# Kernel tuning notes

Hardware: AMD Instinct MI355X
Metric: run time of the kernel (lower is better)

## Reference

```python
import jax, jax.numpy as jnp
import numpy as np

NUM_NODES = 8192
MUL = 64
ENV_P = 6
EPSILON = 1.0 / np.sqrt(17.0)  # 1/sqrt(1 + avg_num_neighbors), avg_num_neighbors=16


def _envelope(u, p=ENV_P):
    # polynomial smoothing envelope (cutoff at u = 1)
    a = -(p + 1) * (p + 2) / 2.0
    b = p * (p + 2)
    c = -p * (p + 1) / 2.0
    f = 1.0 + a * u ** p + b * u ** (p + 1) + c * u ** (p + 2)
    return jnp.where(u < 1.0, f, 0.0)


def setup_inputs() -> dict:
    key = jax.random.key(0)
    ks = jax.random.split(key, 9)
    E, F = 131072, 512
    vectors = jax.random.normal(ks[0], (E, 3), jnp.float32) * 0.35  # mostly inside cutoff
    x = jax.random.normal(ks[1], (E, F), jnp.float32)
    V = jax.random.normal(ks[2], (E, MUL, 4), jnp.float32)  # per mul-channel: [0e | 1o(3)]
    senders = jax.random.randint(ks[3], (E,), 0, NUM_NODES, jnp.int32)
    W_w = jax.random.normal(ks[4], (F, MUL), jnp.float32)
    W1 = jax.random.normal(ks[5], (F + 2 * MUL, 512), jnp.float32)
    W2 = jax.random.normal(ks[6], (512, 512), jnp.float32)
    W3 = jax.random.normal(ks[7], (512, 512), jnp.float32)
    W_lin = jax.random.normal(ks[8], (3 * MUL, MUL), jnp.float32)
    return {"vectors": vectors, "x": x, "V": V, "senders": senders,
            "W_w": W_w, "W1": W1, "W2": W2, "W3": W3, "W_lin": W_lin}


def reference(vectors, x, V, senders, W_w, W1, W2, W3, W_lin):
    E = vectors.shape[0]
    # edge-wise linear producing tensor-product weights  [E, MUL]
    w = (x @ W_w) / np.sqrt(x.shape[-1])
    # spherical harmonics (component norm), l = 0..1 of normalized vectors -> [E, 4]
    r = jnp.linalg.norm(vectors, axis=-1, keepdims=True)          # [E, 1]
    nhat = vectors / r
    Y = jnp.concatenate([jnp.ones((E, 1), vectors.dtype), np.sqrt(3.0) * nhat], axis=1)
    # weighted SH, scatter-sum over senders, gather back (map_back=True), scale by epsilon
    wY_e = w[:, :, None] * Y[:, None, :]                          # [E, MUL, 4]
    agg = jax.ops.segment_sum(wY_e, senders, num_segments=NUM_NODES)
    wY = agg[senders] * EPSILON                                   # [E, MUL, 4]
    # CG tensor product wY (0e+1o) x V (0e+1o), keep 0e and 1o outputs
    a0, a1 = wY[..., 0], wY[..., 1:]
    b0, b1 = V[..., 0], V[..., 1:]
    scal = jnp.concatenate(
        [a0 * b0, jnp.einsum('emi,emi->em', a1, b1) / np.sqrt(3.0)], axis=-1)  # [E, 2*MUL]
    vecs = jnp.concatenate(
        [a0[..., None] * b1, a1 * b0[..., None], jnp.cross(a1, b1) / np.sqrt(2.0)],
        axis=1)                                                   # [E, 3*MUL, 3]
    # concat scalar channel into invariants, 3-layer MLP (silu, linear last)
    xc = jnp.concatenate([x, scal], axis=1)                       # [E, 640]
    h = jax.nn.silu(xc @ W1 / np.sqrt(xc.shape[-1]))
    h = jax.nn.silu(h @ W2 / np.sqrt(h.shape[-1]))
    h = h @ W3 / np.sqrt(h.shape[-1])
    x_out = _envelope(r) * h                                      # [E, 512]
    # equivariant linear over the 1o multiplicity axis
    V_out = jnp.einsum('ekc,km->emc', vecs, W_lin) / np.sqrt(vecs.shape[1])  # [E, MUL, 3]
    return x_out, V_out
```

## Files before the change

kernel.cpp:

```cpp
#include <hip/hip_runtime.h>
#include <cstdint>
#include <cstddef>

#define E_TOT 131072
#define NNODES 8192

typedef __attribute__((ext_vector_type(8))) short bf16x8;
typedef __attribute__((ext_vector_type(4))) float f32x4;
typedef unsigned short u16;
typedef unsigned int u32;

__device__ __forceinline__ u16 f2bf(float f) {
    u32 u = __builtin_bit_cast(u32, f);
    u32 r = (u + 0x7FFFu + ((u >> 16) & 1u)) >> 16;
    return (u16)r;
}

__device__ __forceinline__ void gload16(const u16* g, u16* l) {
    __builtin_amdgcn_global_load_lds((const __attribute__((address_space(1))) void*)g,
                                     (__attribute__((address_space(3))) void*)l, 16, 0, 0);
}

__device__ __forceinline__ bf16x8 lds_frag(const u16* base, int row, int bytecol) {
    return *(const bf16x8*)((const char*)base + row * 128 + (bytecol ^ ((row & 7) << 4)));
}

__global__ void wconv_kernel(const float* __restrict__ src, u16* __restrict__ dst,
                             int K, int N) {
    int idx = blockIdx.x * 256 + threadIdx.x;
    if (idx >= N * K) return;
    int n = idx / K, k = idx - n * K;
    dst[idx] = f2bf(src[(size_t)k * N + n]);
}

__global__ void xconv_kernel(const float4* __restrict__ x, ushort4* __restrict__ xb) {
    size_t i = (size_t)blockIdx.x * 256 + threadIdx.x;
    float4 v = x[i];
    ushort4 o;
    o.x = f2bf(v.x); o.y = f2bf(v.y); o.z = f2bf(v.z); o.w = f2bf(v.w);
    xb[i] = o;
}

__global__ void envy_kernel(const float* __restrict__ vectors, float* __restrict__ env,
                            float4* __restrict__ Y) {
    int e = blockIdx.x * 256 + threadIdx.x;
    float vx = vectors[3 * e + 0], vy = vectors[3 * e + 1], vz = vectors[3 * e + 2];
    float r2 = vx * vx + vy * vy + vz * vz;
    float r = sqrtf(r2);
    float u6 = r2 * r2 * r2;
    float f = 1.0f + u6 * (-28.0f + 48.0f * r - 21.0f * r2);
    env[e] = (r < 1.0f) ? f : 0.0f;
    float inv = 1.7320508075688772f / r;
    Y[e] = make_float4(1.0f, vx * inv, vy * inv, vz * inv);
}

__global__ void hist_kernel(const int* __restrict__ senders, int* __restrict__ cnt) {
    int e = blockIdx.x * 256 + threadIdx.x;
    atomicAdd(&cnt[senders[e]], 1);
}

__launch_bounds__(1024)
__global__ void scan_kernel(const int* __restrict__ cnt, int* __restrict__ off,
                            int* __restrict__ curs) {
    __shared__ int part[1024];
    const int t = threadIdx.x;
    int local[8];
    int s = 0;
#pragma unroll
    for (int j = 0; j < 8; ++j) { local[j] = cnt[t * 8 + j]; s += local[j]; }
    part[t] = s;
    __syncthreads();
    for (int d = 1; d < 1024; d <<= 1) {
        int v = (t >= d) ? part[t - d] : 0;
        __syncthreads();
        part[t] += v;
        __syncthreads();
    }
    int run = part[t] - s;
#pragma unroll
    for (int j = 0; j < 8; ++j) {
        off[t * 8 + j] = run;
        curs[t * 8 + j] = run;
        run += local[j];
    }
    if (t == 1023) off[8192] = run;
}

__global__ void permbuild_kernel(const int* __restrict__ senders, int* __restrict__ curs,
                                 int* __restrict__ perm) {
    int e = blockIdx.x * 256 + threadIdx.x;
    int s = senders[e];
    int p = atomicAdd(&curs[s], 1);
    perm[p] = e;
}

__launch_bounds__(256)
__global__ void gather_kernel(const float* __restrict__ w, const float4* __restrict__ Y,
                              const int* __restrict__ off, const int* __restrict__ perm,
                              float4* __restrict__ agg) {
    const int t = threadIdx.x;
    const int n = blockIdx.x * 4 + (t >> 6);
    const int m = t & 63;
    const int beg = off[n], end = off[n + 1];
    float4 acc = make_float4(0.f, 0.f, 0.f, 0.f);
    for (int i = beg; i < end; ++i) {
        int e = perm[i];
        float wv = w[(size_t)e * 64 + m];
        float4 y = Y[e];
        acc.x += wv * y.x; acc.y += wv * y.y; acc.z += wv * y.z; acc.w += wv * y.w;
    }
    agg[(size_t)n * 64 + m] = acc;
}

__launch_bounds__(256)
__global__ void wgemm_kernel(const u16* __restrict__ XB, const u16* __restrict__ Wt,
                             float* __restrict__ w) {
    __shared__ u16 As[128 * 72];
    __shared__ u16 Bs[64 * 72];
    const int e0 = blockIdx.x * 128;
    const int t = threadIdx.x, lane = t & 63, wid = t >> 6;
    const int lr = lane & 15, lh = lane >> 4;
    const int r8 = t >> 3, c8 = t & 7;
    f32x4 acc[2][4] = {};
    for (int kt = 0; kt < 8; ++kt) {
        const int kk = kt << 6;
#pragma unroll
        for (int i = 0; i < 4; ++i) {
            int row = i * 32 + r8;
            const u16* g = XB + (size_t)(e0 + row) * 512 + kk + c8 * 8;
            *(uint4*)((char*)As + row * 144 + c8 * 16) = *(const uint4*)g;
        }
#pragma unroll
        for (int i = 0; i < 2; ++i) {
            int row = i * 32 + r8;
            const u16* g = Wt + (size_t)row * 512 + kk + c8 * 8;
            *(uint4*)((char*)Bs + row * 144 + c8 * 16) = *(const uint4*)g;
        }
        __syncthreads();
#pragma unroll
        for (int k2 = 0; k2 < 2; ++k2) {
            bf16x8 af[2], bfr[4];
#pragma unroll
            for (int m = 0; m < 2; ++m)
                af[m] = *(const bf16x8*)((const char*)As + (wid * 32 + m * 16 + lr) * 144 + k2 * 64 + lh * 16);
#pragma unroll
            for (int n = 0; n < 4; ++n)
                bfr[n] = *(const bf16x8*)((const char*)Bs + (n * 16 + lr) * 144 + k2 * 64 + lh * 16);
#pragma unroll
            for (int m = 0; m < 2; ++m)
#pragma unroll
                for (int n = 0; n < 4; ++n)
                    acc[m][n] = __builtin_amdgcn_mfma_f32_16x16x32_bf16(af[m], bfr[n], acc[m][n], 0, 0, 0);
        }
        __syncthreads();
    }
    const float s = 0.044194173824159216f;
#pragma unroll
    for (int m = 0; m < 2; ++m)
#pragma unroll
        for (int n = 0; n < 4; ++n)
#pragma unroll
            for (int j = 0; j < 4; ++j) {
                int e = e0 + wid * 32 + m * 16 + lh * 4 + j;
                w[(size_t)e * 64 + n * 16 + lr] = acc[m][n][j] * s;
            }
}

__launch_bounds__(256)
__global__ void edge_kernel(const int* __restrict__ senders, const float4* __restrict__ agg4,
                            const float4* __restrict__ V4, const u16* __restrict__ Wlt,
                            u16* __restrict__ scal, float* __restrict__ Vout) {
    __shared__ u16 a_lds[3][32][200];
    __shared__ u16 w_lds[64 * 200];
    const int t = threadIdx.x;
    const int e0 = blockIdx.x * 32;
#pragma unroll
    for (int i = 0; i < 6; ++i) {
        int c = i * 256 + t;
        int row = c / 24, off = (c % 24) * 8;
        *(uint4*)((char*)w_lds + row * 400 + off * 2) = ((const uint4*)Wlt)[c];
    }
    const float invs3 = 0.5773502691896258f;
    const float invs2 = 0.7071067811865476f;
    const float EPS = 0.24253562503633297f;
#pragma unroll
    for (int i = 0; i < 8; ++i) {
        int el = i * 4 + (t >> 6);
        int m = t & 63;
        int e = e0 + el;
        int s = senders[e];
        float4 a = agg4[(size_t)s * 64 + m];
        a.x *= EPS; a.y *= EPS; a.z *= EPS; a.w *= EPS;
        float4 b = V4[(size_t)e * 64 + m];
        float s0 = a.x * b.x;
        float s1 = (a.y * b.y + a.z * b.z + a.w * b.w) * invs3;
        scal[(size_t)e * 128 + m] = f2bf(s0);
        scal[(size_t)e * 128 + 64 + m] = f2bf(s1);
        float cx = (a.z * b.w - a.w * b.z) * invs2;
        float cy = (a.w * b.y - a.y * b.w) * invs2;
        float cz = (a.y * b.z - a.z * b.y) * invs2;
        a_lds[0][el][m] = f2bf(a.x * b.y);
        a_lds[0][el][64 + m] = f2bf(a.y * b.x);
        a_lds[0][el][128 + m] = f2bf(cx);
        a_lds[1][el][m] = f2bf(a.x * b.z);
        a_lds[1][el][64 + m] = f2bf(a.z * b.x);
        a_lds[1][el][128 + m] = f2bf(cy);
        a_lds[2][el][m] = f2bf(a.x * b.w);
        a_lds[2][el][64 + m] = f2bf(a.w * b.x);
        a_lds[2][el][128 + m] = f2bf(cz);
    }
    __syncthreads();
    const int lane = t & 63, wid = t >> 6;
    const int lr = lane & 15, lh = lane >> 4;
    f32x4 acc[3][2] = {};
    for (int kt = 0; kt < 6; ++kt) {
        bf16x8 bfr = *(const bf16x8*)((const char*)w_lds + (wid * 16 + lr) * 400 + kt * 64 + lh * 16);
#pragma unroll
        for (int c = 0; c < 3; ++c)
#pragma unroll
            for (int m = 0; m < 2; ++m) {
                bf16x8 afr = *(const bf16x8*)((const char*)a_lds + ((c * 32 + m * 16 + lr) * 400) + kt * 64 + lh * 16);
                acc[c][m] = __builtin_amdgcn_mfma_f32_16x16x32_bf16(afr, bfr, acc[c][m], 0, 0, 0);
            }
    }
    __syncthreads();
    float* ot = (float*)a_lds;
    const float sc = 0.07216878364870323f;
#pragma unroll
    for (int c = 0; c < 3; ++c)
#pragma unroll
        for (int m = 0; m < 2; ++m)
#pragma unroll
            for (int j = 0; j < 4; ++j) {
                int row = m * 16 + lh * 4 + j;
                int mul = wid * 16 + lr;
                ot[row * 192 + mul * 3 + c] = acc[c][m][j] * sc;
            }
    __syncthreads();
    float4* vo = (float4*)(Vout + (size_t)e0 * 192);
#pragma unroll
    for (int i = 0; i < 6; ++i)
        vo[i * 256 + t] = ((float4*)ot)[i * 256 + t];
}

template <int MODE>
__launch_bounds__(256)
__global__ void mlp_gemm(const u16* __restrict__ A, const u16* __restrict__ A2,
                         const u16* __restrict__ Bt, const int K, const float scale,
                         const float* __restrict__ env,
                         u16* __restrict__ outb, float* __restrict__ outf) {
    __shared__ u16 As[128 * 64];
    __shared__ u16 Bs[128 * 64];
    const int nwg = gridDim.x;
    const int bid = blockIdx.x;
    const int swz = (bid & 7) * (nwg >> 3) + (bid >> 3);
    const int mt = swz >> 2, nt = swz & 3;
    const int e0 = mt << 7, n0 = nt << 7;
    const int t = threadIdx.x, lane = t & 63, wid = t >> 6;
    const int wm = wid & 1, wn = wid >> 1;
    const int lr = lane & 15, lh = lane >> 4;
    f32x4 acc[4][4] = {};
    const int nkt = K >> 6;
    const int srow = wid * 8 + (lane >> 3);
    const int scol = ((lane & 7) ^ (lane >> 3)) * 8;
    for (int kt = 0; kt < nkt; ++kt) {
        const int kk = kt << 6;
        const int col = kk + scol;
#pragma unroll
        for (int i = 0; i < 4; ++i) {
            const int row = e0 + i * 32 + srow;
            const u16* g;
            if (A2 && kk >= 512) g = A2 + (size_t)row * 128 + (col - 512);
            else                 g = A + (size_t)row * 512 + col;
            gload16(g, As + i * 2048 + wid * 512);
        }
#pragma unroll
        for (int i = 0; i < 4; ++i) {
            const int row = n0 + i * 32 + srow;
            const u16* g = Bt + (size_t)row * K + col;
            gload16(g, Bs + i * 2048 + wid * 512);
        }
        __syncthreads();
#pragma unroll
        for (int k2 = 0; k2 < 2; ++k2) {
            bf16x8 af[4], bfr[4];
#pragma unroll
            for (int m = 0; m < 4; ++m)
                af[m] = lds_frag(As, wm * 64 + m * 16 + lr, k2 * 64 + lh * 16);
#pragma unroll
            for (int n = 0; n < 4; ++n)
                bfr[n] = lds_frag(Bs, wn * 64 + n * 16 + lr, k2 * 64 + lh * 16);
#pragma unroll
            for (int m = 0; m < 4; ++m)
#pragma unroll
                for (int n = 0; n < 4; ++n)
                    acc[m][n] = __builtin_amdgcn_mfma_f32_16x16x32_bf16(af[m], bfr[n], acc[m][n], 0, 0, 0);
        }
        __syncthreads();
    }
#pragma unroll
    for (int m = 0; m < 4; ++m) {
#pragma unroll
        for (int j = 0; j < 4; ++j) {
            const int row = e0 + wm * 64 + m * 16 + lh * 4 + j;
            float ev = (MODE == 1) ? env[row] : 0.0f;
#pragma unroll
            for (int n = 0; n < 4; ++n) {
                const int col = n0 + wn * 64 + n * 16 + lr;
                float v = acc[m][n][j] * scale;
                if (MODE == 0) {
                    float sv = v / (1.0f + __expf(-v));
                    outb[(size_t)row * 512 + col] = f2bf(sv);
                } else {
                    outf[(size_t)row * 512 + col] = v * ev;
                }
            }
        }
    }
}

extern "C" void kernel_launch(void* const* d_in, const int* in_sizes, int n_in,
                              void* d_out, int out_size, void* d_ws, size_t ws_size,
                              hipStream_t stream) {
    const float* vectors = (const float*)d_in[0];
    const float* x       = (const float*)d_in[1];
    const float* V       = (const float*)d_in[2];
    const int*   senders = (const int*)d_in[3];
    const float* W_w     = (const float*)d_in[4];
    const float* W1      = (const float*)d_in[5];
    const float* W2      = (const float*)d_in[6];
    const float* W3      = (const float*)d_in[7];
    const float* W_lin   = (const float*)d_in[8];
    float* out = (float*)d_out;
    char* ws = (char*)d_ws;

    u16*    XB   = (u16*)(ws + 0x0);
    u16*    H1   = (u16*)(ws + 0x8000000);
    u16*    SCAL = (u16*)(ws + 0x10000000);
    float*  AGG  = (float*)(ws + 0x12000000);
    float*  ENV  = (float*)(ws + 0x12800000);
    float4* Yb   = (float4*)(ws + 0x12880000);
    float*  Wbuf = (float*)(ws + 0x12A80000);
    u16*    WT   = (u16*)(ws + 0x14A80000);
    u16* Wwt = WT;
    u16* W1t = Wwt + 64 * 512;
    u16* W2t = W1t + 512 * 640;
    u16* W3t = W2t + 512 * 512;
    u16* Wlt = W3t + 512 * 512;
    u16* H2 = XB;
    int* COUNT = (int*)(ws + 0x15000000);
    int* OFF   = (int*)(ws + 0x15010000);
    int* CURS  = (int*)(ws + 0x15020000);
    int* PERM  = (int*)(ws + 0x15030000);

    hipMemsetAsync(COUNT, 0, NNODES * sizeof(int), stream);

    wconv_kernel<<<(64 * 512) / 256, 256, 0, stream>>>(W_w, Wwt, 512, 64);
    wconv_kernel<<<(512 * 640) / 256, 256, 0, stream>>>(W1, W1t, 640, 512);
    wconv_kernel<<<(512 * 512) / 256, 256, 0, stream>>>(W2, W2t, 512, 512);
    wconv_kernel<<<(512 * 512) / 256, 256, 0, stream>>>(W3, W3t, 512, 512);
    wconv_kernel<<<(64 * 192) / 256, 256, 0, stream>>>(W_lin, Wlt, 192, 64);

    xconv_kernel<<<(E_TOT * 512 / 4) / 256, 256, 0, stream>>>((const float4*)x, (ushort4*)XB);
    envy_kernel<<<E_TOT / 256, 256, 0, stream>>>(vectors, ENV, Yb);

    hist_kernel<<<E_TOT / 256, 256, 0, stream>>>(senders, COUNT);
    scan_kernel<<<1, 1024, 0, stream>>>(COUNT, OFF, CURS);
    permbuild_kernel<<<E_TOT / 256, 256, 0, stream>>>(senders, CURS, PERM);

    wgemm_kernel<<<E_TOT / 128, 256, 0, stream>>>(XB, Wwt, Wbuf);
    gather_kernel<<<NNODES / 4, 256, 0, stream>>>(Wbuf, Yb, OFF, PERM, (float4*)AGG);

    edge_kernel<<<E_TOT / 32, 256, 0, stream>>>(senders, (const float4*)AGG, (const float4*)V,
                                                Wlt, SCAL, out + (size_t)E_TOT * 512);

    const float s640 = 0.03952847075210474f;
    const float s512 = 0.044194173824159216f;
    mlp_gemm<0><<<(E_TOT / 128) * 4, 256, 0, stream>>>(XB, SCAL, W1t, 640, s640, nullptr, H1, nullptr);
    mlp_gemm<0><<<(E_TOT / 128) * 4, 256, 0, stream>>>(H1, nullptr, W2t, 512, s512, nullptr, H2, nullptr);
    mlp_gemm<1><<<(E_TOT / 128) * 4, 256, 0, stream>>>(H2, nullptr, W3t, 512, s512, ENV, nullptr, out);
}
```

Before: 650.8 us.

## Use 256x256 double-buffered tiles with 512 threads in MLP GEMMs

The three MLP GEMMs move from 128x128 tiles with 256 threads to 256x256 tiles with 512 threads (8 waves, each computing 128x64). LDS is double-buffered so the global-to-LDS loads for the next k-tile are issued before the MFMAs on the current one, leaving one barrier per iteration. The larger tile improves operand reuse and cuts global traffic per FLOP. In exchange it uses 128KB of LDS and 128 accumulator floats per lane, so occupancy drops, and the grid shrinks to 1024 blocks.

```diff
diff --git a/kernel.cpp b/kernel.cpp
--- a/kernel.cpp
+++ b/kernel.cpp
@@ -244,54 +244,71 @@
 }
 
 template <int MODE>
-__launch_bounds__(256)
+__launch_bounds__(512, 2)
 __global__ void mlp_gemm(const u16* __restrict__ A, const u16* __restrict__ A2,
                          const u16* __restrict__ Bt, const int K, const float scale,
                          const float* __restrict__ env,
                          u16* __restrict__ outb, float* __restrict__ outf) {
-    __shared__ u16 As[128 * 64];
-    __shared__ u16 Bs[128 * 64];
+    __shared__ u16 lds[2][2][256 * 64];
     const int nwg = gridDim.x;
     const int bid = blockIdx.x;
     const int swz = (bid & 7) * (nwg >> 3) + (bid >> 3);
-    const int mt = swz >> 2, nt = swz & 3;
-    const int e0 = mt << 7, n0 = nt << 7;
+    const int mt = swz >> 1, nt = swz & 1;
+    const int e0 = mt << 8, n0 = nt << 8;
     const int t = threadIdx.x, lane = t & 63, wid = t >> 6;
-    const int wm = wid & 1, wn = wid >> 1;
+    const int wm = wid >> 2, wn = wid & 3;
     const int lr = lane & 15, lh = lane >> 4;
-    f32x4 acc[4][4] = {};
+    const int sr8 = lane >> 3;
+    const int scol = ((lane & 7) ^ sr8) << 3;
+    f32x4 acc[8][4] = {};
     const int nkt = K >> 6;
-    const int srow = wid * 8 + (lane >> 3);
-    const int scol = ((lane & 7) ^ (lane >> 3)) * 8;
+
     for (int kt = 0; kt < nkt; ++kt) {
-        const int kk = kt << 6;
-        const int col = kk + scol;
-#pragma unroll
-        for (int i = 0; i < 4; ++i) {
-            const int row = e0 + i * 32 + srow;
-            const u16* g;
-            if (A2 && kk >= 512) g = A2 + (size_t)row * 128 + (col - 512);
-            else                 g = A + (size_t)row * 512 + col;
-            gload16(g, As + i * 2048 + wid * 512);
-        }
-#pragma unroll
-        for (int i = 0; i < 4; ++i) {
-            const int row = n0 + i * 32 + srow;
-            const u16* g = Bt + (size_t)row * K + col;
-            gload16(g, Bs + i * 2048 + wid * 512);
-        }
-        __syncthreads();
+        if (kt == 0) {
+            const int col = scol;
+#pragma unroll
+            for (int i = 0; i < 4; ++i) {
+                const int row = e0 + i * 64 + wid * 8 + sr8;
+                gload16(A + (size_t)row * 512 + col, &lds[0][0][i * 4096 + wid * 512]);
+            }
+#pragma unroll
+            for (int i = 0; i < 4; ++i) {
+                const int row = n0 + i * 64 + wid * 8 + sr8;
+                gload16(Bt + (size_t)row * K + col, &lds[0][1][i * 4096 + wid * 512]);
+            }
+            __syncthreads();
+        }
+        if (kt + 1 < nkt) {
+            const int kk = (kt + 1) << 6;
+            const int col = kk + scol;
+            const int nb = (kt + 1) & 1;
+#pragma unroll
+            for (int i = 0; i < 4; ++i) {
+                const int row = e0 + i * 64 + wid * 8 + sr8;
+                const u16* g;
+                if (A2 && kk >= 512) g = A2 + (size_t)row * 128 + (col - 512);
+                else                 g = A + (size_t)row * 512 + col;
+                gload16(g, &lds[nb][0][i * 4096 + wid * 512]);
+            }
+#pragma unroll
+            for (int i = 0; i < 4; ++i) {
+                const int row = n0 + i * 64 + wid * 8 + sr8;
+                gload16(Bt + (size_t)row * K + col, &lds[nb][1][i * 4096 + wid * 512]);
+            }
+        }
+        const u16* Ab = lds[kt & 1][0];
+        const u16* Bb = lds[kt & 1][1];
 #pragma unroll
         for (int k2 = 0; k2 < 2; ++k2) {
-            bf16x8 af[4], bfr[4];
-#pragma unroll
-            for (int m = 0; m < 4; ++m)
-                af[m] = lds_frag(As, wm * 64 + m * 16 + lr, k2 * 64 + lh * 16);
+            bf16x8 af[8], bfr[4];
+#pragma unroll
+            for (int m = 0; m < 8; ++m)
+                af[m] = lds_frag(Ab, wm * 128 + m * 16 + lr, k2 * 64 + lh * 16);
 #pragma unroll
             for (int n = 0; n < 4; ++n)
-                bfr[n] = lds_frag(Bs, wn * 64 + n * 16 + lr, k2 * 64 + lh * 16);
-#pragma unroll
-            for (int m = 0; m < 4; ++m)
+                bfr[n] = lds_frag(Bb, wn * 64 + n * 16 + lr, k2 * 64 + lh * 16);
+#pragma unroll
+            for (int m = 0; m < 8; ++m)
 #pragma unroll
                 for (int n = 0; n < 4; ++n)
                     acc[m][n] = __builtin_amdgcn_mfma_f32_16x16x32_bf16(af[m], bfr[n], acc[m][n], 0, 0, 0);
@@ -299,10 +316,10 @@
         __syncthreads();
     }
 #pragma unroll
-    for (int m = 0; m < 4; ++m) {
+    for (int m = 0; m < 8; ++m) {
 #pragma unroll
         for (int j = 0; j < 4; ++j) {
-            const int row = e0 + wm * 64 + m * 16 + lh * 4 + j;
+            const int row = e0 + wm * 128 + m * 16 + lh * 4 + j;
             float ev = (MODE == 1) ? env[row] : 0.0f;
 #pragma unroll
             for (int n = 0; n < 4; ++n) {
@@ -376,7 +393,8 @@
 
     const float s640 = 0.03952847075210474f;
     const float s512 = 0.044194173824159216f;
-    mlp_gemm<0><<<(E_TOT / 128) * 4, 256, 0, stream>>>(XB, SCAL, W1t, 640, s640, nullptr, H1, nullptr);
-    mlp_gemm<0><<<(E_TOT / 128) * 4, 256, 0, stream>>>(H1, nullptr, W2t, 512, s512, nullptr, H2, nullptr);
-    mlp_gemm<1><<<(E_TOT / 128) * 4, 256, 0, stream>>>(H2, nullptr, W3t, 512, s512, ENV, nullptr, out);
-}
+    const int gemm_grid = (E_TOT / 256) * 2;
+    mlp_gemm<0><<<gemm_grid, 512, 0, stream>>>(XB, SCAL, W1t, 640, s640, nullptr, H1, nullptr);
+    mlp_gemm<0><<<gemm_grid, 512, 0, stream>>>(H1, nullptr, W2t, 512, s512, nullptr, H2, nullptr);
+    mlp_gemm<1><<<gemm_grid, 512, 0, stream>>>(H2, nullptr, W3t, 512, s512, ENV, nullptr, out);
+}
```

Result: faster. 600.9 us (-7.7%).
